# Optimization experiments

Measured on AMD Instinct MI355X. Metric: run time of the kernel, lower is better.

The kernel has to match this reference:

```python
import jax, jax.numpy as jnp
from jax import lax
import numpy as np

INPUT_SIZE, HIDDEN, NUM_LAYERS, NUM_CLASSES = 128, 256, 2, 100
B, T = 256, 512


def _lstm_layer(x, W_ih, W_hh, b_ih, b_hh):
    # x: [B, T, in]; W_ih: [4H, in]; W_hh: [4H, H]; gate order i,f,g,o (PyTorch)
    Bsz = x.shape[0]
    H = W_hh.shape[1]
    x_proj = jnp.einsum('bti,gi->btg', x, W_ih) + b_ih + b_hh  # [B, T, 4H]
    h0 = jnp.zeros((Bsz, H), x.dtype)
    c0 = jnp.zeros((Bsz, H), x.dtype)

    def step(carry, xt):
        h, c = carry
        gates = xt + h @ W_hh.T  # [B, 4H]
        i, f, g, o = jnp.split(gates, 4, axis=-1)
        i = jax.nn.sigmoid(i)
        f = jax.nn.sigmoid(f)
        g = jnp.tanh(g)
        o = jax.nn.sigmoid(o)
        c = f * c + i * g
        h = o * jnp.tanh(c)
        return (h, c), h

    _, hs = lax.scan(step, (h0, c0), jnp.swapaxes(x_proj, 0, 1))  # hs: [T, B, H]
    return jnp.swapaxes(hs, 0, 1)  # [B, T, H]


def setup_inputs() -> dict:
    key = jax.random.key(0)
    ks = jax.random.split(key, 12)
    s_in = 1.0 / np.sqrt(HIDDEN)
    inp = {
        'x': jax.random.normal(ks[0], (B, T, INPUT_SIZE), jnp.float32),
        'W_ih0': jax.random.uniform(ks[1], (4 * HIDDEN, INPUT_SIZE), jnp.float32, -s_in, s_in),
        'W_hh0': jax.random.uniform(ks[2], (4 * HIDDEN, HIDDEN), jnp.float32, -s_in, s_in),
        'b_ih0': jax.random.uniform(ks[3], (4 * HIDDEN,), jnp.float32, -s_in, s_in),
        'b_hh0': jax.random.uniform(ks[4], (4 * HIDDEN,), jnp.float32, -s_in, s_in),
        'W_ih1': jax.random.uniform(ks[5], (4 * HIDDEN, HIDDEN), jnp.float32, -s_in, s_in),
        'W_hh1': jax.random.uniform(ks[6], (4 * HIDDEN, HIDDEN), jnp.float32, -s_in, s_in),
        'b_ih1': jax.random.uniform(ks[7], (4 * HIDDEN,), jnp.float32, -s_in, s_in),
        'b_hh1': jax.random.uniform(ks[8], (4 * HIDDEN,), jnp.float32, -s_in, s_in),
        'fc_w': jax.random.uniform(ks[9], (NUM_CLASSES, HIDDEN), jnp.float32, -s_in, s_in),
        'fc_b': jax.random.uniform(ks[10], (NUM_CLASSES,), jnp.float32, -s_in, s_in),
    }
    return inp


def reference(x, W_ih0, W_hh0, b_ih0, b_hh0, W_ih1, W_hh1, b_ih1, b_hh1, fc_w, fc_b):
    h = _lstm_layer(x, W_ih0, W_hh0, b_ih0, b_hh0)
    h = _lstm_layer(h, W_ih1, W_hh1, b_ih1, b_hh1)
    return h[:, -1, :] @ fc_w.T + fc_b  # [B, num_classes]
```

## Files before the change

kernel.cpp:

```cpp
#include <hip/hip_runtime.h>
#include <math.h>

namespace {

constexpr int kB  = 256;
constexpr int kT  = 512;
constexpr int kIn = 128;
constexpr int kH  = 256;
constexpr int kG  = 1024;
constexpr int kNC = 100;
constexpr int kCT = 64;
constexpr int kNCh = kT / kCT;

typedef __bf16 bf16x8 __attribute__((ext_vector_type(8)));
typedef float f32x4 __attribute__((ext_vector_type(4)));
typedef int i32x4 __attribute__((ext_vector_type(4)));
typedef unsigned short u16;
static_assert(sizeof(bf16x8) == 16, "bf16x8 must be 4 VGPRs");

__device__ __forceinline__ float sigm(float x) {
  return __builtin_amdgcn_rcpf(1.0f + __expf(-x));
}
__device__ __forceinline__ float tanh_f(float x) {
  const float e = __expf(-2.0f * x);
  return (1.0f - e) * __builtin_amdgcn_rcpf(1.0f + e);
}
__device__ __forceinline__ u16 f2bf(float f) {
  return __builtin_bit_cast(u16, (__bf16)f);
}
__device__ __forceinline__ float bf2f(u16 v) {
  return __builtin_bit_cast(float, ((unsigned)v) << 16);
}

__device__ __forceinline__ void glds16(const void* g, void* l) {
  __builtin_amdgcn_global_load_lds(
      (const __attribute__((address_space(1))) void*)g,
      (__attribute__((address_space(3))) void*)l, 16, 0, 0);
}
__device__ __forceinline__ void glds16_llc(const void* g, void* l) {
  __builtin_amdgcn_global_load_lds(
      (const __attribute__((address_space(1))) void*)g,
      (__attribute__((address_space(3))) void*)l, 16, 0, 17);
}
__device__ __forceinline__ void st_bf16_llc(u16* p, u16 v) {
  asm volatile("global_store_short %0, %1, off sc0 sc1"
               :: "v"((unsigned long long)(uintptr_t)p), "v"(v) : "memory");
}
__device__ __forceinline__ void st_i32_llc(int* p, int v) {
  asm volatile("global_store_dword %0, %1, off sc0 sc1"
               :: "v"((unsigned long long)(uintptr_t)p), "v"(v) : "memory");
}
__device__ __forceinline__ int poll16_min(const int* p) {
  i32x4 a, b, c, d;
  asm volatile(
      "global_load_dwordx4 %0, %4, off sc0 sc1\n\t"
      "global_load_dwordx4 %1, %5, off sc0 sc1\n\t"
      "global_load_dwordx4 %2, %6, off sc0 sc1\n\t"
      "global_load_dwordx4 %3, %7, off sc0 sc1\n\t"
      "s_waitcnt vmcnt(0)"
      : "=&v"(a), "=&v"(b), "=&v"(c), "=&v"(d)
      : "v"((unsigned long long)(uintptr_t)p),
        "v"((unsigned long long)(uintptr_t)(p + 4)),
        "v"((unsigned long long)(uintptr_t)(p + 8)),
        "v"((unsigned long long)(uintptr_t)(p + 12))
      : "memory");
  int m = a.x;
  m = min(m, a.y); m = min(m, a.z); m = min(m, a.w);
  m = min(m, b.x); m = min(m, b.y); m = min(m, b.z); m = min(m, b.w);
  m = min(m, c.x); m = min(m, c.y); m = min(m, c.z); m = min(m, c.w);
  m = min(m, d.x); m = min(m, d.y); m = min(m, d.z); m = min(m, d.w);
  return m;
}

__global__ __launch_bounds__(256) void pack_whh_frag(
    const float* __restrict__ whh, u16* __restrict__ wpk) {
  const int idx = blockIdx.x * 256 + threadIdx.x;
  const int e  = idx & 7;
  const int l  = (idx >> 3) & 63;
  const int kb = (idx >> 9) & 7;
  const int g  = (idx >> 12) & 3;
  const int wv = idx >> 14;
  const int n = (g << 8) | (wv << 4) | (l & 15);
  const int k = (kb << 5) | (((l >> 4) & 3) << 3) | e;
  wpk[idx] = f2bf(whh[n * kH + k]);
}

template <int K>
__global__ __launch_bounds__(256) void pack_wih_frag(
    const float* __restrict__ w, u16* __restrict__ wp) {
  constexpr int kbBits = (K == 128) ? 2 : 3;
  const int idx = blockIdx.x * 256 + threadIdx.x;
  const int e  = idx & 7;
  const int l  = (idx >> 3) & 63;
  const int kb = (idx >> 9) & ((K / 32) - 1);
  const int n16 = idx >> (9 + kbBits);
  const int n = (n16 << 4) | (l & 15);
  const int k = (kb << 5) | (((l >> 4) & 3) << 3) | e;
  wp[idx] = f2bf(w[n * K + k]);
}

__global__ __launch_bounds__(256) void conv_x(
    const float* __restrict__ x, u16* __restrict__ xbf) {
  const int f4 = blockIdx.x * 256 + threadIdx.x;
  const int rowid = f4 >> 5;
  const int c4 = f4 & 31;
  const int b = rowid >> 9, t = rowid & 511;
  const float4 v = reinterpret_cast<const float4*>(x)[f4];
  ushort4 o;
  o.x = f2bf(v.x); o.y = f2bf(v.y); o.z = f2bf(v.z); o.w = f2bf(v.w);
  reinterpret_cast<ushort4*>(xbf)[(t * 256 + b) * 32 + c4] = o;
}

template <int K>
__device__ __forceinline__ void gemm_body(
    const u16* __restrict__ A, const u16* __restrict__ Bp,
    const float* __restrict__ b1, const float* __restrict__ b2,
    u16* __restrict__ P2, int gbid, unsigned char* smem) {
  constexpr int NKB = K / 32;
  const int g = gbid & 3, mt = gbid >> 2;
  const int tt = mt >> 2, bq = mt & 3;
  const int tid = threadIdx.x, w = tid >> 6, l = tid & 63;

  u16* albuf = (u16*)smem;
  u16* bbuf  = (u16*)(smem + 8192);
  u16* sout  = (u16*)smem;

  const u16* Ab = A + ((size_t)(tt * 256 + bq * 64 + w * 16 + (l & 15))) * K +
                  ((l >> 4) & 3) * 8;
  const u16* Bb = Bp + ((size_t)((g * 16 + w * 4) * NKB) * 64 + l) * 8;

  float bb[4];
#pragma unroll
  for (int j = 0; j < 4; ++j) {
    const int n = g * 256 + (w * 4 + j) * 16 + (l & 15);
    bb[j] = b1[n] + b2[n];
  }

  f32x4 acc[4][4];
#pragma unroll
  for (int mf = 0; mf < 4; ++mf)
#pragma unroll
    for (int nf = 0; nf < 4; ++nf) acc[mf][nf] = f32x4{0.f, 0.f, 0.f, 0.f};

#define STAGE(kb, buf)                                                     \
  {                                                                        \
    glds16(Ab + (kb) * 32, albuf + ((buf) * 4 + w) * 512);                 \
    _Pragma("unroll") for (int j = 0; j < 4; ++j)                          \
        glds16(Bb + ((size_t)(j * NKB + (kb)) * 64) * 8,                   \
               bbuf + ((buf) * 16 + w * 4 + j) * 512);                     \
  }

  STAGE(0, 0);
#pragma unroll
  for (int kb = 0; kb < NKB; ++kb) {
    __syncthreads();
    if (kb + 1 < NKB) STAGE(kb + 1, (kb + 1) & 1);
    const int buf = kb & 1;
    bf16x8 af[4], bf[4];
#pragma unroll
    for (int mf = 0; mf < 4; ++mf)
      af[mf] = *reinterpret_cast<const bf16x8*>(albuf + (buf * 4 + mf) * 512 + l * 8);
#pragma unroll
    for (int nf = 0; nf < 4; ++nf)
      bf[nf] = *reinterpret_cast<const bf16x8*>(bbuf + (buf * 16 + w * 4 + nf) * 512 + l * 8);
#pragma unroll
    for (int mf = 0; mf < 4; ++mf)
#pragma unroll
      for (int nf = 0; nf < 4; ++nf)
        acc[mf][nf] = __builtin_amdgcn_mfma_f32_16x16x32_bf16(
            af[mf], bf[nf], acc[mf][nf], 0, 0, 0);
  }
#undef STAGE

  __syncthreads();
#pragma unroll
  for (int mf = 0; mf < 4; ++mf)
#pragma unroll
    for (int nf = 0; nf < 4; ++nf) {
      ushort4 p;
      p.x = f2bf(acc[mf][nf][0] + bb[nf]);
      p.y = f2bf(acc[mf][nf][1] + bb[nf]);
      p.z = f2bf(acc[mf][nf][2] + bb[nf]);
      p.w = f2bf(acc[mf][nf][3] + bb[nf]);
      *reinterpret_cast<ushort4*>(
          sout + (mf * 16 + w * 4 + nf) * 256 + (l & 15) * 16 + ((l >> 4) & 3) * 4) = p;
    }
  __syncthreads();
#pragma unroll
  for (int i = 0; i < 8; ++i) {
    const int chunk = i * 8 + (tid >> 5);
    const int mf = chunk >> 4, wc = chunk & 15;
    const size_t dst =
        ((((size_t)(bq * 4 + mf) * 64 + tt) * 16 + wc) * 4 + g) * 256 +
        (tid & 31) * 8;
    *reinterpret_cast<uint4*>(P2 + dst) =
        *reinterpret_cast<const uint4*>(sout + (mf * 16 + wc) * 256 + (tid & 31) * 8);
  }
}

template <int K>
__global__ __launch_bounds__(256, 4) void gemm_flat(
    const u16* __restrict__ A, const u16* __restrict__ Bp,
    const float* __restrict__ b1, const float* __restrict__ b2,
    u16* __restrict__ P2) {
  __shared__ __align__(16) unsigned char smem[40960];
  gemm_body<K>(A, Bp, b1, b2, P2, blockIdx.x, smem);
}

__global__ __launch_bounds__(256, 1) void fused_step(
    const u16* __restrict__ P2_0, const u16* __restrict__ wpk_0,
    float* __restrict__ cs_0, u16* __restrict__ Ho_0, float* __restrict__ hl_0,
    u16* __restrict__ hx_0, int* __restrict__ tg_0, int first_0,
    const u16* __restrict__ P2_1, const u16* __restrict__ wpk_1,
    float* __restrict__ cs_1, u16* __restrict__ Ho_1, float* __restrict__ hl_1,
    u16* __restrict__ hx_1, int* __restrict__ tg_1, int first_1,
    const u16* __restrict__ Ag, const u16* __restrict__ Bg,
    const float* __restrict__ b1g, const float* __restrict__ b2g,
    u16* __restrict__ Pg) {
  __shared__ __align__(16) unsigned char smem[40960];

  if (blockIdx.x >= 128) {
    if (Ag) gemm_body<kIn>(Ag, Bg, b1g, b2g, Pg, blockIdx.x - 128, smem);
    return;
  }

  const int role = blockIdx.x >> 6;
  const u16* P2  = role ? P2_1 : P2_0;
  if (!P2) return;
  const u16* wpk = role ? wpk_1 : wpk_0;
  float* cstate  = role ? cs_1 : cs_0;
  u16* HoutBf    = role ? Ho_1 : Ho_0;
  float* hlast   = role ? hl_1 : hl_0;
  u16* hx        = role ? hx_1 : hx_0;
  int* tags      = role ? tg_1 : tg_0;
  const int first = role ? first_1 : first_0;

  const int bid6 = blockIdx.x & 63;
  const int tid = threadIdx.x;
  const int ug = tid >> 6;
  const int l  = tid & 63;
  const int bblk = bid6 & 15;
  const int hs   = bid6 >> 4;
  const int R0 = bblk << 4;
  const int wv16 = (hs << 2) | ug;
  const int jj = (wv16 << 4) | (l & 15);
  const int mg = ((l >> 4) & 3) << 2;
  const int rowb = R0 + mg;

  u16 (*albuf)[8][512] = reinterpret_cast<u16 (*)[8][512]>(smem);

  int* tgb = tags + bblk * 1024;
  u16* hx0 = hx;
  u16* hx1 = hx + (size_t)kB * kH;

  bf16x8 wr[4][8];
#pragma unroll
  for (int g = 0; g < 4; ++g)
#pragma unroll
    for (int kb = 0; kb < 8; ++kb) {
      wr[g][kb] = *reinterpret_cast<const bf16x8*>(
          wpk + (size_t)(((wv16 * 4 + g) * 8 + kb) * 64 + l) * 8);
      asm volatile("" : "+v"(wr[g][kb]));
    }

  f32x4 c4;
  float hnew[4];
  if (first) {
#pragma unroll
    for (int r = 0; r < 4; ++r) c4[r] = 0.f;
  } else {
#pragma unroll
    for (int r = 0; r < 4; ++r) c4[r] = cstate[(rowb + r) * kH + jj];
  }

  const u16* __restrict__ Pb =
      P2 + ((size_t)bblk * 64 * 16 + wv16) * 1024 + ((l & 15) << 4) + mg;
  ushort4 pf[4];
#pragma unroll
  for (int g = 0; g < 4; ++g)
    pf[g] = *reinterpret_cast<const ushort4*>(Pb + (g << 8));

  const int gkb = ug << 1;
#define ISSUE_GLDS(buf, bsel)                                               \
  {                                                                         \
    _Pragma("unroll") for (int q = 0; q < 2; ++q) {                         \
      const int kb = gkb + q;                                               \
      glds16_llc((buf) + ((size_t)(R0 + (l & 15))) * 256 + kb * 32 +        \
                     ((l >> 4) & 3) * 8,                                    \
                 &albuf[bsel][kb][0]);                                      \
    }                                                                       \
  }

  ISSUE_GLDS(hx0, 0);

  for (int tt = 0; tt < kCT; ++tt) {
    __syncthreads();

    f32x4 acc[4];
#pragma unroll
    for (int g = 0; g < 4; ++g) {
      acc[g][0] = bf2f(pf[g].x);
      acc[g][1] = bf2f(pf[g].y);
      acc[g][2] = bf2f(pf[g].z);
      acc[g][3] = bf2f(pf[g].w);
    }
    if (tt + 1 < kCT) {
#pragma unroll
      for (int g = 0; g < 4; ++g)
        pf[g] = *reinterpret_cast<const ushort4*>(
            Pb + (size_t)(tt + 1) * 16384 + (g << 8));
    }

    const u16* ab = &albuf[tt & 1][0][0];
#pragma unroll
    for (int kb = 0; kb < 8; ++kb) {
      const bf16x8 a = *reinterpret_cast<const bf16x8*>(ab + kb * 512 + l * 8);
      acc[0] = __builtin_amdgcn_mfma_f32_16x16x32_bf16(a, wr[0][kb], acc[0], 0, 0, 0);
      acc[1] = __builtin_amdgcn_mfma_f32_16x16x32_bf16(a, wr[1][kb], acc[1], 0, 0, 0);
      acc[2] = __builtin_amdgcn_mfma_f32_16x16x32_bf16(a, wr[2][kb], acc[2], 0, 0, 0);
      acc[3] = __builtin_amdgcn_mfma_f32_16x16x32_bf16(a, wr[3][kb], acc[3], 0, 0, 0);
    }

#pragma unroll
    for (int r = 0; r < 4; ++r) {
      const float ig = sigm(acc[0][r]);
      const float fg = sigm(acc[1][r]);
      const float gg = tanh_f(acc[2][r]);
      const float og = sigm(acc[3][r]);
      const float cc = fg * c4[r] + ig * gg;
      c4[r] = cc;
      hnew[r] = og * tanh_f(cc);
    }

    u16* hw = ((tt + 1) & 1) ? hx1 : hx0;
#pragma unroll
    for (int r = 0; r < 4; ++r)
      st_bf16_llc(hw + ((size_t)(rowb + r) << 8) + jj, f2bf(hnew[r]));

    if (tt + 1 < kCT) {
      const int want = tt + 1;
      asm volatile("s_waitcnt vmcnt(0)" ::: "memory");
      if (l == 0) st_i32_llc(tgb + want * 16 + (hs * 4 + ug), want);
      if (HoutBf) {
#pragma unroll
        for (int r = 0; r < 4; ++r)
          HoutBf[((size_t)tt * 256 + rowb + r) * 256 + jj] = f2bf(hnew[r]);
      }
      while (poll16_min(tgb + want * 16) < want)
        __builtin_amdgcn_s_sleep(1);
      const u16* hr = ((tt + 1) & 1) ? hx1 : hx0;
      ISSUE_GLDS(hr, (tt + 1) & 1);
    } else {
      if (HoutBf) {
#pragma unroll
        for (int r = 0; r < 4; ++r)
          HoutBf[((size_t)tt * 256 + rowb + r) * 256 + jj] = f2bf(hnew[r]);
      }
      if (hlast) {
#pragma unroll
        for (int r = 0; r < 4; ++r)
          hlast[(rowb + r) * kH + jj] = hnew[r];
      }
    }
  }
#undef ISSUE_GLDS

#pragma unroll
  for (int r = 0; r < 4; ++r) cstate[(rowb + r) * kH + jj] = c4[r];
}

__global__ __launch_bounds__(128) void fc_kernel(
    const float* __restrict__ hlast, const float* __restrict__ fcw,
    const float* __restrict__ fcb, float* __restrict__ out) {
  const int b = blockIdx.x;
  const int n = threadIdx.x;
  __shared__ float sh[kH];
  sh[n] = hlast[b * kH + n];
  sh[n + 128] = hlast[b * kH + n + 128];
  __syncthreads();
  if (n < kNC) {
    float a = fcb[n];
    const float* wrow = fcw + n * kH;
#pragma unroll 8
    for (int k = 0; k < kH; ++k) a += sh[k] * wrow[k];
    out[b * kNC + n] = a;
  }
}

}

extern "C" void kernel_launch(void* const* d_in, const int* in_sizes, int n_in,
                              void* d_out, int out_size, void* d_ws, size_t ws_size,
                              hipStream_t stream) {
  (void)in_sizes; (void)n_in; (void)out_size; (void)ws_size;
  const float* x    = (const float*)d_in[0];
  const float* Wih0 = (const float*)d_in[1];
  const float* Whh0 = (const float*)d_in[2];
  const float* bih0 = (const float*)d_in[3];
  const float* bhh0 = (const float*)d_in[4];
  const float* Wih1 = (const float*)d_in[5];
  const float* Whh1 = (const float*)d_in[6];
  const float* bih1 = (const float*)d_in[7];
  const float* bhh1 = (const float*)d_in[8];
  const float* fcw  = (const float*)d_in[9];
  const float* fcb  = (const float*)d_in[10];
  float* out = (float*)d_out;

  char* base = (char*)d_ws;
  size_t off = 0;
  auto take = [&](size_t sz) { char* p = base + off; off += (sz + 255) & ~(size_t)255; return p; };
  const size_t szP2   = (size_t)kB * kCT * kG * 2;
  const size_t szXbf  = (size_t)kT * kB * kIn * 2;
  const size_t szH0   = (size_t)kCT * kB * kH * 2;
  const size_t szC    = (size_t)kB * kH * 4;
  const size_t szHx   = (size_t)2 * kB * kH * 2;
  const size_t szWih0 = (size_t)64 * (kIn / 32) * 512 * 2;
  const size_t szWih1 = (size_t)64 * (kH / 32) * 512 * 2;
  const size_t szWhh  = (size_t)262144 * 2;
  const size_t szTags = (size_t)16 * 16 * 1024 * 4;

  u16* P2a0 = (u16*)take(szP2);
  u16* P2a1 = (u16*)take(szP2);
  u16* P2b  = (u16*)take(szP2);
  u16* xbf  = (u16*)take(szXbf);
  u16* H0bf = (u16*)take(szH0);
  float* c0s = (float*)take(szC);
  float* c1s = (float*)take(szC);
  float* h1s = (float*)take(szC);
  u16* hxA = (u16*)take(szHx);
  u16* hxB = (u16*)take(szHx);
  u16* WpIh0 = (u16*)take(szWih0);
  u16* WpIh1 = (u16*)take(szWih1);
  u16* Wpk0 = (u16*)take(szWhh);
  u16* Wpk1 = (u16*)take(szWhh);
  int* tags = (int*)take(szTags);

  hipMemsetAsync(tags, 0, szTags, stream);
  hipMemsetAsync(hxA, 0, szHx, stream);
  hipMemsetAsync(hxB, 0, szHx, stream);

  conv_x<<<dim3(16384), dim3(256), 0, stream>>>(x, xbf);
  pack_wih_frag<kIn><<<dim3(512), dim3(256), 0, stream>>>(Wih0, WpIh0);
  pack_wih_frag<kH><<<dim3(1024), dim3(256), 0, stream>>>(Wih1, WpIh1);
  pack_whh_frag<<<dim3(1024), dim3(256), 0, stream>>>(Whh0, Wpk0);
  pack_whh_frag<<<dim3(1024), dim3(256), 0, stream>>>(Whh1, Wpk1);

  auto tslot = [&](int s) { return tags + (size_t)s * 16 * 1024; };
  auto p2a = [&](int ch) { return (ch & 1) ? P2a1 : P2a0; };
  const size_t ckElems = (size_t)kCT * kB * kIn;

  gemm_flat<kIn><<<dim3(1024), dim3(256), 0, stream>>>(
      xbf, WpIh0, bih0, bhh0, P2a0);

  fused_step<<<dim3(1152), dim3(256), 0, stream>>>(
      P2a0, Wpk0, c0s, H0bf, nullptr, hxA, tslot(0), 1,
      nullptr, nullptr, nullptr, nullptr, nullptr, nullptr, nullptr, 0,
      xbf + ckElems, WpIh0, bih0, bhh0, P2a1);

  for (int ch = 1; ch < kNCh; ++ch) {
    gemm_flat<kH><<<dim3(1024), dim3(256), 0, stream>>>(
        H0bf, WpIh1, bih1, bhh1, P2b);
    const bool haveG = (ch + 1 < kNCh);
    const u16* gA = haveG ? xbf + (size_t)(ch + 1) * ckElems : nullptr;
    u16* gP = haveG ? p2a(ch + 1) : nullptr;
    const int grid = haveG ? 1152 : 128;
    fused_step<<<dim3(grid), dim3(256), 0, stream>>>(
        p2a(ch), Wpk0, c0s, H0bf, nullptr, hxA, tslot(2 * ch), 0,
        P2b, Wpk1, c1s, nullptr, h1s, hxB, tslot(2 * (ch - 1) + 1),
        (ch == 1) ? 1 : 0,
        gA, WpIh0, bih0, bhh0, gP);
  }

  gemm_flat<kH><<<dim3(1024), dim3(256), 0, stream>>>(
      H0bf, WpIh1, bih1, bhh1, P2b);
  fused_step<<<dim3(128), dim3(256), 0, stream>>>(
      nullptr, nullptr, nullptr, nullptr, nullptr, nullptr, nullptr, 0,
      P2b, Wpk1, c1s, nullptr, h1s, hxB, tslot(2 * (kNCh - 1) + 1), 0,
      nullptr, nullptr, nullptr, nullptr, nullptr);
  fc_kernel<<<dim3(kB), dim3(128), 0, stream>>>(h1s, fcw, fcb, out);
}
```

Before: 1.817 ms.

## Fuse layer-1 input GEMM into persistent step kernel with per-timestep readiness flags

Removes the separate per-chunk layer-1 input-projection GEMM launch and runs it inside the fused step kernel as extra blocks. Those blocks write P2b with LLC-coherent stores and publish per-timestep done flags, which the layer-1 recurrence polls before prefetching each timestep's gate preactivations. The layer-0 hidden output is double-buffered so the GEMM can read chunk ch-1 while layer 0 writes chunk ch. This aims to overlap the GEMM with the recurrence and cut launch serialization. The cost is extra polling, coherent-load overhead, and the risk of deadlock if the GEMM blocks are not co-scheduled with the recurrence blocks.

```diff
diff --git a/kernel.cpp b/kernel.cpp
--- a/kernel.cpp
+++ b/kernel.cpp
@@ -11,6 +11,7 @@
 constexpr int kNC = 100;
 constexpr int kCT = 64;
 constexpr int kNCh = kT / kCT;
+constexpr int kGdStride = 1280;
 
 typedef __bf16 bf16x8 __attribute__((ext_vector_type(8)));
 typedef float f32x4 __attribute__((ext_vector_type(4)));
@@ -48,6 +49,10 @@
 }
 __device__ __forceinline__ void st_i32_llc(int* p, int v) {
   asm volatile("global_store_dword %0, %1, off sc0 sc1"
+               :: "v"((unsigned long long)(uintptr_t)p), "v"(v) : "memory");
+}
+__device__ __forceinline__ void st_i4_llc(void* p, i32x4 v) {
+  asm volatile("global_store_dwordx4 %0, %1, off sc0 sc1"
                :: "v"((unsigned long long)(uintptr_t)p), "v"(v) : "memory");
 }
 __device__ __forceinline__ int poll16_min(const int* p) {
@@ -71,6 +76,20 @@
   m = min(m, d.x); m = min(m, d.y); m = min(m, d.z); m = min(m, d.w);
   return m;
 }
+__device__ __forceinline__ void pf_issue_llc(const u16* p,
+                                             unsigned long long pf[4]) {
+  asm volatile(
+      "global_load_dwordx2 %0, %4, off sc0 sc1\n\t"
+      "global_load_dwordx2 %1, %5, off sc0 sc1\n\t"
+      "global_load_dwordx2 %2, %6, off sc0 sc1\n\t"
+      "global_load_dwordx2 %3, %7, off sc0 sc1"
+      : "=&v"(pf[0]), "=&v"(pf[1]), "=&v"(pf[2]), "=&v"(pf[3])
+      : "v"((unsigned long long)(uintptr_t)p),
+        "v"((unsigned long long)(uintptr_t)(p + 256)),
+        "v"((unsigned long long)(uintptr_t)(p + 512)),
+        "v"((unsigned long long)(uintptr_t)(p + 768))
+      : "memory");
+}
 
 __global__ __launch_bounds__(256) void pack_whh_frag(
     const float* __restrict__ whh, u16* __restrict__ wpk) {
@@ -115,7 +134,7 @@
 __device__ __forceinline__ void gemm_body(
     const u16* __restrict__ A, const u16* __restrict__ Bp,
     const float* __restrict__ b1, const float* __restrict__ b2,
-    u16* __restrict__ P2, int gbid, unsigned char* smem) {
+    u16* __restrict__ P2, int gbid, unsigned char* smem, int* gflag) {
   constexpr int NKB = K / 32;
   const int g = gbid & 3, mt = gbid >> 2;
   const int tt = mt >> 2, bq = mt & 3;
@@ -193,8 +212,19 @@
     const size_t dst =
         ((((size_t)(bq * 4 + mf) * 64 + tt) * 16 + wc) * 4 + g) * 256 +
         (tid & 31) * 8;
-    *reinterpret_cast<uint4*>(P2 + dst) =
-        *reinterpret_cast<const uint4*>(sout + (mf * 16 + wc) * 256 + (tid & 31) * 8);
+    const i32x4 val =
+        *reinterpret_cast<const i32x4*>(sout + (mf * 16 + wc) * 256 + (tid & 31) * 8);
+    if (gflag) st_i4_llc(P2 + dst, val);
+    else       *reinterpret_cast<i32x4*>(P2 + dst) = val;
+  }
+  if (gflag) {
+    asm volatile("s_waitcnt vmcnt(0)" ::: "memory");
+    __syncthreads();
+    if (tid == 0) {
+      st_i32_llc(gflag + tt * 16 + ((g << 2) | bq), 1);
+      __hip_atomic_fetch_add(gflag + 1024, 1, __ATOMIC_RELAXED,
+                             __HIP_MEMORY_SCOPE_AGENT);
+    }
   }
 }
 
@@ -204,23 +234,32 @@
     const float* __restrict__ b1, const float* __restrict__ b2,
     u16* __restrict__ P2) {
   __shared__ __align__(16) unsigned char smem[40960];
-  gemm_body<K>(A, Bp, b1, b2, P2, blockIdx.x, smem);
+  gemm_body<K>(A, Bp, b1, b2, P2, blockIdx.x, smem, nullptr);
 }
 
 __global__ __launch_bounds__(256, 1) void fused_step(
     const u16* __restrict__ P2_0, const u16* __restrict__ wpk_0,
-    float* __restrict__ cs_0, u16* __restrict__ Ho_0, float* __restrict__ hl_0,
+    float* __restrict__ cs_0, u16* __restrict__ Ho_0,
     u16* __restrict__ hx_0, int* __restrict__ tg_0, int first_0,
     const u16* __restrict__ P2_1, const u16* __restrict__ wpk_1,
-    float* __restrict__ cs_1, u16* __restrict__ Ho_1, float* __restrict__ hl_1,
+    float* __restrict__ cs_1, float* __restrict__ hl_1,
     u16* __restrict__ hx_1, int* __restrict__ tg_1, int first_1,
-    const u16* __restrict__ Ag, const u16* __restrict__ Bg,
-    const float* __restrict__ b1g, const float* __restrict__ b2g,
-    u16* __restrict__ Pg) {
+    int* __restrict__ gd1,
+    const u16* __restrict__ A1, u16* __restrict__ P1,
+    const u16* __restrict__ B1g, const float* __restrict__ b11,
+    const float* __restrict__ b21,
+    const u16* __restrict__ Ag, u16* __restrict__ Pg,
+    const u16* __restrict__ B0g, const float* __restrict__ b10,
+    const float* __restrict__ b20) {
   __shared__ __align__(16) unsigned char smem[40960];
 
+  if (blockIdx.x >= 1152) {
+    if (Ag) gemm_body<kIn>(Ag, B0g, b10, b20, Pg, blockIdx.x - 1152, smem,
+                           nullptr);
+    return;
+  }
   if (blockIdx.x >= 128) {
-    if (Ag) gemm_body<kIn>(Ag, Bg, b1g, b2g, Pg, blockIdx.x - 128, smem);
+    if (A1) gemm_body<kH>(A1, B1g, b11, b21, P1, blockIdx.x - 128, smem, gd1);
     return;
   }
 
@@ -229,10 +268,11 @@
   if (!P2) return;
   const u16* wpk = role ? wpk_1 : wpk_0;
   float* cstate  = role ? cs_1 : cs_0;
-  u16* HoutBf    = role ? Ho_1 : Ho_0;
-  float* hlast   = role ? hl_1 : hl_0;
+  u16* HoutBf    = role ? nullptr : Ho_0;
+  float* hlast   = role ? hl_1 : nullptr;
   u16* hx        = role ? hx_1 : hx_0;
   int* tags      = role ? tg_1 : tg_0;
+  int* gdone     = role ? gd1 : nullptr;
   const int first = role ? first_1 : first_0;
 
   const int bid6 = blockIdx.x & 63;
@@ -273,12 +313,22 @@
     for (int r = 0; r < 4; ++r) c4[r] = cstate[(rowb + r) * kH + jj];
   }
 
+  bool alldone = (gdone == nullptr);
+  auto gate = [&](int t) {
+    if (alldone) return;
+    if (__hip_atomic_load(gdone + 1024, __ATOMIC_RELAXED,
+                          __HIP_MEMORY_SCOPE_AGENT) >= 1024) {
+      alldone = true;
+      return;
+    }
+    while (poll16_min(gdone + t * 16) < 1) __builtin_amdgcn_s_sleep(1);
+  };
+
   const u16* __restrict__ Pb =
       P2 + ((size_t)bblk * 64 * 16 + wv16) * 1024 + ((l & 15) << 4) + mg;
-  ushort4 pf[4];
-#pragma unroll
-  for (int g = 0; g < 4; ++g)
-    pf[g] = *reinterpret_cast<const ushort4*>(Pb + (g << 8));
+  unsigned long long pfq[4];
+  gate(0);
+  pf_issue_llc(Pb, pfq);
 
   const int gkb = ug << 1;
 #define ISSUE_GLDS(buf, bsel)                                               \
@@ -295,20 +345,21 @@
 
   for (int tt = 0; tt < kCT; ++tt) {
     __syncthreads();
+    __builtin_amdgcn_sched_barrier(0);
 
     f32x4 acc[4];
 #pragma unroll
     for (int g = 0; g < 4; ++g) {
-      acc[g][0] = bf2f(pf[g].x);
-      acc[g][1] = bf2f(pf[g].y);
-      acc[g][2] = bf2f(pf[g].z);
-      acc[g][3] = bf2f(pf[g].w);
-    }
-    if (tt + 1 < kCT) {
-#pragma unroll
-      for (int g = 0; g < 4; ++g)
-        pf[g] = *reinterpret_cast<const ushort4*>(
-            Pb + (size_t)(tt + 1) * 16384 + (g << 8));
+      const ushort4 u = __builtin_bit_cast(ushort4, pfq[g]);
+      acc[g][0] = bf2f(u.x);
+      acc[g][1] = bf2f(u.y);
+      acc[g][2] = bf2f(u.z);
+      acc[g][3] = bf2f(u.w);
+    }
+    const bool more = (tt + 1 < kCT);
+    if (more) {
+      gate(tt + 1);
+      pf_issue_llc(Pb + (size_t)(tt + 1) * 16384, pfq);
     }
 
     const u16* ab = &albuf[tt & 1][0][0];
@@ -337,10 +388,10 @@
     for (int r = 0; r < 4; ++r)
       st_bf16_llc(hw + ((size_t)(rowb + r) << 8) + jj, f2bf(hnew[r]));
 
-    if (tt + 1 < kCT) {
+    if (more) {
       const int want = tt + 1;
       asm volatile("s_waitcnt vmcnt(0)" ::: "memory");
-      if (l == 0) st_i32_llc(tgb + want * 16 + (hs * 4 + ug), want);
+      if (l == 0) st_i32_llc(tgb + want * 16 + wv16, want);
       if (HoutBf) {
 #pragma unroll
         for (int r = 0; r < 4; ++r)
@@ -418,12 +469,14 @@
   const size_t szWih1 = (size_t)64 * (kH / 32) * 512 * 2;
   const size_t szWhh  = (size_t)262144 * 2;
   const size_t szTags = (size_t)16 * 16 * 1024 * 4;
+  const size_t szGd   = (size_t)8 * kGdStride * 4;
 
   u16* P2a0 = (u16*)take(szP2);
   u16* P2a1 = (u16*)take(szP2);
   u16* P2b  = (u16*)take(szP2);
   u16* xbf  = (u16*)take(szXbf);
-  u16* H0bf = (u16*)take(szH0);
+  u16* H0a  = (u16*)take(szH0);
+  u16* H0b  = (u16*)take(szH0);
   float* c0s = (float*)take(szC);
   float* c1s = (float*)take(szC);
   float* h1s = (float*)take(szC);
@@ -434,8 +487,10 @@
   u16* Wpk0 = (u16*)take(szWhh);
   u16* Wpk1 = (u16*)take(szWhh);
   int* tags = (int*)take(szTags);
+  int* gd   = (int*)take(szGd);
 
   hipMemsetAsync(tags, 0, szTags, stream);
+  hipMemsetAsync(gd, 0, szGd, stream);
   hipMemsetAsync(hxA, 0, szHx, stream);
   hipMemsetAsync(hxB, 0, szHx, stream);
 
@@ -446,36 +501,37 @@
   pack_whh_frag<<<dim3(1024), dim3(256), 0, stream>>>(Whh1, Wpk1);
 
   auto tslot = [&](int s) { return tags + (size_t)s * 16 * 1024; };
+  auto gslot = [&](int s) { return gd + (size_t)s * kGdStride; };
   auto p2a = [&](int ch) { return (ch & 1) ? P2a1 : P2a0; };
+  auto h0p = [&](int ch) { return (ch & 1) ? H0b : H0a; };
   const size_t ckElems = (size_t)kCT * kB * kIn;
 
   gemm_flat<kIn><<<dim3(1024), dim3(256), 0, stream>>>(
       xbf, WpIh0, bih0, bhh0, P2a0);
 
+  fused_step<<<dim3(2176), dim3(256), 0, stream>>>(
+      P2a0, Wpk0, c0s, H0a, hxA, tslot(0), 1,
+      nullptr, nullptr, nullptr, nullptr, nullptr, nullptr, 0, nullptr,
+      nullptr, nullptr, nullptr, nullptr, nullptr,
+      xbf + ckElems, P2a1, WpIh0, bih0, bhh0);
+
+  for (int ch = 1; ch < kNCh; ++ch) {
+    const bool haveG0 = (ch + 1 < kNCh);
+    fused_step<<<dim3(2176), dim3(256), 0, stream>>>(
+        p2a(ch), Wpk0, c0s, h0p(ch), hxA, tslot(2 * ch), 0,
+        P2b, Wpk1, c1s, h1s, hxB, tslot(2 * (ch - 1) + 1),
+        (ch == 1) ? 1 : 0, gslot(ch - 1),
+        h0p(ch - 1), P2b, WpIh1, bih1, bhh1,
+        haveG0 ? xbf + (size_t)(ch + 1) * ckElems : nullptr,
+        haveG0 ? p2a(ch + 1) : nullptr, WpIh0, bih0, bhh0);
+  }
+
   fused_step<<<dim3(1152), dim3(256), 0, stream>>>(
-      P2a0, Wpk0, c0s, H0bf, nullptr, hxA, tslot(0), 1,
-      nullptr, nullptr, nullptr, nullptr, nullptr, nullptr, nullptr, 0,
-      xbf + ckElems, WpIh0, bih0, bhh0, P2a1);
-
-  for (int ch = 1; ch < kNCh; ++ch) {
-    gemm_flat<kH><<<dim3(1024), dim3(256), 0, stream>>>(
-        H0bf, WpIh1, bih1, bhh1, P2b);
-    const bool haveG = (ch + 1 < kNCh);
-    const u16* gA = haveG ? xbf + (size_t)(ch + 1) * ckElems : nullptr;
-    u16* gP = haveG ? p2a(ch + 1) : nullptr;
-    const int grid = haveG ? 1152 : 128;
-    fused_step<<<dim3(grid), dim3(256), 0, stream>>>(
-        p2a(ch), Wpk0, c0s, H0bf, nullptr, hxA, tslot(2 * ch), 0,
-        P2b, Wpk1, c1s, nullptr, h1s, hxB, tslot(2 * (ch - 1) + 1),
-        (ch == 1) ? 1 : 0,
-        gA, WpIh0, bih0, bhh0, gP);
-  }
-
-  gemm_flat<kH><<<dim3(1024), dim3(256), 0, stream>>>(
-      H0bf, WpIh1, bih1, bhh1, P2b);
-  fused_step<<<dim3(128), dim3(256), 0, stream>>>(
-      nullptr, nullptr, nullptr, nullptr, nullptr, nullptr, nullptr, 0,
-      P2b, Wpk1, c1s, nullptr, h1s, hxB, tslot(2 * (kNCh - 1) + 1), 0,
+      nullptr, nullptr, nullptr, nullptr, nullptr, nullptr, 0,
+      P2b, Wpk1, c1s, h1s, hxB, tslot(2 * (kNCh - 1) + 1), 0,
+      gslot(kNCh - 1),
+      h0p(kNCh - 1), P2b, WpIh1, bih1, bhh1,
       nullptr, nullptr, nullptr, nullptr, nullptr);
+
   fc_kernel<<<dim3(kB), dim3(128), 0, stream>>>(h1s, fcw, fcb, out);
 }
```

Result: no change. 1.835 ms (+1.0%).
